# Kernel optimization log

Measured on AMD Instinct MI355X. Metric: run time of the kernel, lower is better.

Reference implementation:

```python
import jax, jax.numpy as jnp
import numpy as np

B, C, H, W = 8, 128, 64, 64
C8, C2 = C // 8, C // 2


def conv1x1(x, w, b):
    # x: [B,Cin,H,W], w: [Cout,Cin], b: [Cout]
    return jnp.einsum('bchw,oc->bohw', x, w) + b[None, :, None, None]


def maxpool2(x):
    # 2x2 stride-2 max pool on [B,C,H,W]
    b, c, h, w = x.shape
    return x.reshape(b, c, h // 2, 2, w // 2, 2).max(axis=(3, 5))


def setup_inputs() -> dict:
    key = jax.random.key(0)
    ks = jax.random.split(key, 10)
    s_in = 1.0 / np.sqrt(C)
    s_c2 = 1.0 / np.sqrt(C2)
    return {
        'x': jax.random.normal(ks[0], (B, C, H, W), dtype=jnp.float32),
        'w_theta': jax.random.uniform(ks[1], (C8, C), jnp.float32, -s_in, s_in),
        'b_theta': jax.random.uniform(ks[2], (C8,), jnp.float32, -s_in, s_in),
        'w_phi': jax.random.uniform(ks[3], (C8, C), jnp.float32, -s_in, s_in),
        'b_phi': jax.random.uniform(ks[4], (C8,), jnp.float32, -s_in, s_in),
        'w_g': jax.random.uniform(ks[5], (C2, C), jnp.float32, -s_in, s_in),
        'b_g': jax.random.uniform(ks[6], (C2,), jnp.float32, -s_in, s_in),
        'w_attn': jax.random.uniform(ks[7], (C, C2), jnp.float32, -s_c2, s_c2),
        'b_attn': jax.random.uniform(ks[8], (C,), jnp.float32, -s_c2, s_c2),
        'sigma': jnp.zeros((1,), dtype=jnp.float32),
    }


def reference(x, w_theta, b_theta, w_phi, b_phi, w_g, b_g, w_attn, b_attn, sigma):
    b, ch, h, w = x.shape
    n, m = h * w, (h * w) // 4
    theta = conv1x1(x, w_theta, b_theta).reshape(b, ch // 8, n)          # [B,C8,N]
    phi = maxpool2(conv1x1(x, w_phi, b_phi)).reshape(b, ch // 8, m)      # [B,C8,M]
    attn = jax.nn.softmax(jnp.einsum('bdn,bdm->bnm', theta, phi), axis=-1)  # [B,N,M]
    g = maxpool2(conv1x1(x, w_g, b_g)).reshape(b, ch // 2, m)            # [B,C2,M]
    attn_g = jnp.einsum('bcm,bnm->bcn', g, attn).reshape(b, ch // 2, h, w)
    attn_g = conv1x1(attn_g, w_attn, b_attn)
    return x + sigma[0] * attn_g
```

## Files before the change

### kernel.cpp

```cpp
#include <hip/hip_runtime.h>
#include <hip/hip_bf16.h>
#include <math.h>
#include <string.h>

#define Bn 8
#define Cn 128
#define Nn 4096
#define Mn 1024
#define C8n 16
#define C2n 64

typedef __attribute__((ext_vector_type(8))) short short8;
typedef __attribute__((ext_vector_type(4))) float floatx4;
typedef __attribute__((ext_vector_type(4))) unsigned short ushortx4;

__device__ __forceinline__ unsigned short f2bf(float f) {
    union { float f; unsigned u; } v; v.f = f;
    unsigned r = v.u + 0x7fff + ((v.u >> 16) & 1);
    return (unsigned short)(r >> 16);
}
__device__ __forceinline__ unsigned pk2(float a, float b) {
    __hip_bfloat162 h = __float22bfloat162_rn(make_float2(a, b));
    union { __hip_bfloat162 h2; unsigned u; } cv;
    cv.h2 = h;
    return cv.u;
}

__global__ __launch_bounds__(256) void k1_pre(
    const float* __restrict__ x,
    const float* __restrict__ w_theta, const float* __restrict__ b_theta,
    const float* __restrict__ w_phi,   const float* __restrict__ b_phi,
    const float* __restrict__ w_g,     const float* __restrict__ b_g,
    unsigned short* __restrict__ thA,
    unsigned short* __restrict__ phB,
    unsigned short* __restrict__ gB)
{
    __shared__ unsigned short wA[6 * 4 * 64 * 8];
    __shared__ unsigned short xB[8 * 4 * 64 * 8];
    __shared__ unsigned short pool[80][33];
    __shared__ float biases[96];

    const int t    = threadIdx.x;
    const int b    = blockIdx.x & 7;
    const int h2   = blockIdx.x >> 3;
    const int wv   = t >> 6;
    const int lane = t & 63;
    const int q    = lane >> 4;
    const int l15  = lane & 15;
    const float L2E = 1.4426950408889634f;

    if (t < 96)
        biases[t] = (t < 16) ? b_theta[t] * L2E
                  : (t < 32) ? b_phi[t - 16] : b_g[t - 32];

    #pragma unroll
    for (int k = 0; k < 12; ++k) {
        int u  = t + k * 256;
        int oc = u >> 5, c4 = u & 31;
        const float* src = (oc < 16) ? (w_theta + oc * Cn)
                         : (oc < 32) ? (w_phi + (oc - 16) * Cn)
                                     : (w_g + (oc - 32) * Cn);
        float4 wv4 = *(const float4*)(src + c4 * 4);
        float sc = (oc < 16) ? L2E : 1.f;
        int c = c4 * 4;
        int ot = oc >> 4, kc = c >> 5, qq = (c >> 3) & 3, jj = c & 7;
        uint2 pk = { pk2(wv4.x * sc, wv4.y * sc), pk2(wv4.z * sc, wv4.w * sc) };
        *(uint2*)(wA + (((ot * 4 + kc) * 64 + qq * 16 + (oc & 15)) * 8 + jj)) = pk;
    }

    const float* xb = x + (size_t)b * Cn * Nn + h2 * 128;
    #pragma unroll
    for (int k = 0; k < 16; ++k) {
        int u   = t + k * 256;
        int pos = u & 127, c4 = u >> 7;
        int c   = c4 * 4;
        float v0 = xb[(size_t)(c + 0) * Nn + pos];
        float v1 = xb[(size_t)(c + 1) * Nn + pos];
        float v2 = xb[(size_t)(c + 2) * Nn + pos];
        float v3 = xb[(size_t)(c + 3) * Nn + pos];
        int pt = pos >> 4, kc = c >> 5, qq = (c >> 3) & 3, jj = c & 7;
        uint2 pk = { pk2(v0, v1), pk2(v2, v3) };
        *(uint2*)(xB + (((pt * 4 + kc) * 64 + qq * 16 + (pos & 15)) * 8 + jj)) = pk;
    }
    __syncthreads();

    floatx4 acc[6][2];
    #pragma unroll
    for (int ot = 0; ot < 6; ++ot)
        #pragma unroll
        for (int p2 = 0; p2 < 2; ++p2) acc[ot][p2] = (floatx4){0.f, 0.f, 0.f, 0.f};

    #pragma unroll
    for (int kc = 0; kc < 4; ++kc) {
        short8 Bf0 = *(const short8*)(xB + ((wv * 4 + kc) * 64 + lane) * 8);
        short8 Bf1 = *(const short8*)(xB + (((wv + 4) * 4 + kc) * 64 + lane) * 8);
        #pragma unroll
        for (int ot = 0; ot < 6; ++ot) {
            short8 Af = *(const short8*)(wA + ((ot * 4 + kc) * 64 + lane) * 8);
            acc[ot][0] = __builtin_amdgcn_mfma_f32_16x16x32_bf16(Af, Bf0, acc[ot][0], 0, 0, 0);
            acc[ot][1] = __builtin_amdgcn_mfma_f32_16x16x32_bf16(Af, Bf1, acc[ot][1], 0, 0, 0);
        }
    }

    #pragma unroll
    for (int p2 = 0; p2 < 2; ++p2) {
        const int pt = wv + p2 * 4;
        float v0 = acc[0][p2][0] + biases[q * 4 + 0];
        float v1 = acc[0][p2][1] + biases[q * 4 + 1];
        float v2 = acc[0][p2][2] + biases[q * 4 + 2];
        float v3 = acc[0][p2][3] + biases[q * 4 + 3];
        uint2 pk = { pk2(v0, v1), pk2(v2, v3) };
        *(uint2*)(thA + ((((size_t)b * 256 + h2 * 8 + pt) * 2 + (q >> 1)) * 128
                         + l15 * 8 + (q & 1) * 4)) = pk;
    }

    #pragma unroll
    for (int ot = 1; ot < 6; ++ot) {
        #pragma unroll
        for (int r = 0; r < 4; ++r) {
            float vmax = fmaxf(acc[ot][0][r], acc[ot][1][r]);
            float pmax = fmaxf(vmax, __shfl_xor(vmax, 1, 64));
            if ((l15 & 1) == 0) {
                int oc = (ot - 1) * 16 + q * 4 + r;
                int w2 = wv * 8 + (l15 >> 1);
                pool[oc][w2] = f2bf(pmax + biases[16 + oc]);
            }
        }
    }
    __syncthreads();

    if (t < 64) {
        int w2h = t >> 5, ml = (t >> 1) & 15, dh = t & 1;
        int w2 = w2h * 16 + ml;
        ushortx4 lo, hi;
        #pragma unroll
        for (int j = 0; j < 4; ++j) { lo[j] = pool[dh * 8 + j][w2];
                                      hi[j] = pool[dh * 8 + 4 + j][w2]; }
        unsigned short* dst = phB + (((size_t)b * 64 + h2 * 2 + w2h) * 2 + dh) * 128 + ml * 8;
        *(ushortx4*)dst = lo;
        *(ushortx4*)(dst + 4) = hi;
    }
    {
        int c = t >> 2, sq = t & 3;
        ushortx4 lo, hi;
        #pragma unroll
        for (int j = 0; j < 8; ++j) {
            int w2 = (j & 1) * 16 + sq * 4 + (j >> 1);
            unsigned short v = pool[16 + c][w2];
            if (j < 4) lo[j] = v; else hi[j - 4] = v;
        }
        unsigned short* dst = gB + ((((size_t)b * 32 + h2) * 4 + (c >> 4)) * 4 + sq) * 128
                              + (c & 15) * 8;
        *(ushortx4*)dst = lo;
        *(ushortx4*)(dst + 4) = hi;
    }
}

__global__ __launch_bounds__(256, 2) void k2_attn(
    const float* __restrict__ x,
    const unsigned short* __restrict__ thA,
    const unsigned short* __restrict__ phB,
    const unsigned short* __restrict__ gB,
    const float* __restrict__ w_attn, const float* __restrict__ b_attn,
    const float* __restrict__ sigma_p,
    float* __restrict__ out)
{
    __shared__ float smem[18816];
    unsigned short* phis = (unsigned short*)smem;
    unsigned short* gs   = (unsigned short*)smem + 4096;
    char* Pall = (char*)smem + 40960;
    float* battn = (float*)((char*)smem + 74752);

    const int tid  = threadIdx.x;
    const int wave = tid >> 6;
    const int lane = tid & 63;
    const int q    = lane >> 4;
    const int l15  = lane & 15;
    const int b    = blockIdx.x & 7;
    const int n0   = (blockIdx.x >> 3) * 64;
    const int nw   = n0 + wave * 16;
    char* Pbase = Pall + wave * 8448;

    const float sg = sigma_p[0];

    short8 thf = {};
    if (q < 2)
        thf = *(const short8*)(thA + ((((size_t)b * 256 + (nw >> 4)) * 2 + q) * 16 + l15) * 8);

    floatx4 O[4];
    #pragma unroll
    for (int cs = 0; cs < 4; ++cs) O[cs] = (floatx4){0.f, 0.f, 0.f, 0.f};
    float L[4] = {0.f, 0.f, 0.f, 0.f};

    const float4* phib = (const float4*)(phB + (size_t)b * 64 * 256);
    const float4* gbb  = (const float4*)(gB + (size_t)b * 32 * 2048);

    float4 pre[10];
    #pragma unroll
    for (int k = 0; k < 10; ++k) {
        int i = tid + k * 256;
        pre[k] = (i < 512) ? phib[i] : gbb[i - 512];
    }

    for (int s = 0; s < 4; ++s) {
        __syncthreads();
        #pragma unroll
        for (int k = 0; k < 10; ++k) {
            int i = tid + k * 256;
            if (i < 512) ((float4*)smem)[i] = pre[k];
            else ((float4*)((char*)smem + 8192))[i - 512] = pre[k];
        }
        __syncthreads();
        if (s < 3) {
            #pragma unroll
            for (int k = 0; k < 10; ++k) {
                int i = tid + k * 256;
                pre[k] = (i < 512) ? phib[(s + 1) * 512 + i]
                                   : gbb[(s + 1) * 2048 + (i - 512)];
            }
        }

        #pragma unroll
        for (int g2 = 0; g2 < 8; ++g2) {
            short8 bf0 = {}, bf1 = {};
            if (q < 2) {
                bf0 = *(const short8*)(phis + (((2 * g2)     * 2 + q) * 16 + l15) * 8);
                bf1 = *(const short8*)(phis + (((2 * g2 + 1) * 2 + q) * 16 + l15) * 8);
            }
            floatx4 S0 = __builtin_amdgcn_mfma_f32_16x16x32_bf16(
                             thf, bf0, (floatx4){0.f, 0.f, 0.f, 0.f}, 0, 0, 0);
            floatx4 S1 = __builtin_amdgcn_mfma_f32_16x16x32_bf16(
                             thf, bf1, (floatx4){0.f, 0.f, 0.f, 0.f}, 0, 0, 0);
            #pragma unroll
            for (int r = 0; r < 4; ++r) {
                float pa = exp2f(S0[r]);
                float pb = exp2f(S1[r]);
                L[r] += pa + pb;
                *(unsigned*)(Pbase + (q * 4 + r) * 528 + g2 * 64 + l15 * 4) = pk2(pa, pb);
            }
        }

        #pragma unroll
        for (int ch = 0; ch < 8; ++ch) {
            short8 Af = *(const short8*)(Pbase + l15 * 528 + ch * 64 + q * 16);
            const unsigned short* gchunk = gs + ch * 2048;
            #pragma unroll
            for (int cs = 0; cs < 4; ++cs) {
                short8 Bf = *(const short8*)(gchunk + ((cs * 4 + q) * 16 + l15) * 8);
                O[cs] = __builtin_amdgcn_mfma_f32_16x16x32_bf16(Af, Bf, O[cs], 0, 0, 0);
            }
        }
    }

    #pragma unroll
    for (int d = 1; d <= 8; d <<= 1)
        #pragma unroll
        for (int r = 0; r < 4; ++r) L[r] += __shfl_xor(L[r], d, 64);

    __syncthreads();
    {
        unsigned short* wAe = (unsigned short*)smem;
        #pragma unroll
        for (int k = 0; k < 8; ++k) {
            int i = tid + k * 256;
            float4 wv = ((const float4*)w_attn)[i];
            int o = i >> 4, c = (i & 15) * 4;
            uint2 pk = { pk2(wv.x, wv.y), pk2(wv.z, wv.w) };
            *(uint2*)(wAe + ((o >> 4) * 2 + (c >> 5)) * 512 + (o & 15) * 32 + (c & 31)) = pk;
        }
        if (tid < 128) battn[tid] = b_attn[tid];
    }
    {
        float inv[4];
        #pragma unroll
        for (int r = 0; r < 4; ++r) inv[r] = 1.0f / L[r];
        unsigned short* Ob = (unsigned short*)Pbase;
        #pragma unroll
        for (int cs = 0; cs < 4; ++cs)
            #pragma unroll
            for (int r = 0; r < 4; ++r)
                Ob[(q * 4 + r) * 72 + cs * 16 + l15] = f2bf(O[cs][r] * inv[r]);
    }
    __syncthreads();

    {
        unsigned short* wAe = (unsigned short*)smem;
        unsigned short* Ob = (unsigned short*)Pbase;
        short8 B0 = *(const short8*)(Ob + l15 * 72 + q * 8);
        short8 B1 = *(const short8*)(Ob + l15 * 72 + 32 + q * 8);
        const float* xw = x   + (size_t)b * Cn * Nn + nw + l15;
        float*       ow = out + (size_t)b * Cn * Nn + nw + l15;
        #pragma unroll
        for (int ot = 0; ot < 8; ++ot) {
            short8 A0 = *(const short8*)(wAe + (ot * 2 + 0) * 512 + l15 * 32 + q * 8);
            short8 A1 = *(const short8*)(wAe + (ot * 2 + 1) * 512 + l15 * 32 + q * 8);
            floatx4 D = __builtin_amdgcn_mfma_f32_16x16x32_bf16(
                            A0, B0, (floatx4){0.f, 0.f, 0.f, 0.f}, 0, 0, 0);
            D = __builtin_amdgcn_mfma_f32_16x16x32_bf16(A1, B1, D, 0, 0, 0);
            #pragma unroll
            for (int r = 0; r < 4; ++r) {
                int o = ot * 16 + q * 4 + r;
                float v = D[r] + battn[o];
                ow[(size_t)o * Nn] = xw[(size_t)o * Nn] + sg * v;
            }
        }
    }
}

extern "C" void kernel_launch(void* const* d_in, const int* in_sizes, int n_in,
                              void* d_out, int out_size, void* d_ws, size_t ws_size,
                              hipStream_t stream) {
    const float* x       = (const float*)d_in[0];
    const float* w_theta = (const float*)d_in[1];
    const float* b_theta = (const float*)d_in[2];
    const float* w_phi   = (const float*)d_in[3];
    const float* b_phi   = (const float*)d_in[4];
    const float* w_g     = (const float*)d_in[5];
    const float* b_g     = (const float*)d_in[6];
    const float* w_attn  = (const float*)d_in[7];
    const float* b_attn  = (const float*)d_in[8];
    const float* sigma   = (const float*)d_in[9];
    float* out = (float*)d_out;

    unsigned short* thA = (unsigned short*)d_ws;
    unsigned short* phB = thA + 524288;
    unsigned short* gBp = phB + 131072;

    k1_pre<<<256, 256, 0, stream>>>(x, w_theta, b_theta, w_phi, b_phi,
                                    w_g, b_g, thA, phB, gBp);
    k2_attn<<<512, 256, 0, stream>>>(x, thA, phB, gBp, w_attn, b_attn, sigma, out);
}
```

Measured before the change: 129.9 us.

## Double-buffer phi/g tiles via direct global-to-LDS loads with smaller stages

Replaces the register-staged prefetch (global to registers, then a store to LDS) with __builtin_amdgcn_global_load_lds into two alternating LDS buffers. The M loop runs in 8 stages of 128 columns instead of 4 of 256, and the P scratch per wave shrinks to match. This removes the register pressure of the ten float4 prefetch registers and the second barrier per stage, and overlaps the next tile's load with compute. In exchange there are more loop iterations and barriers in total. There is no explicit vmcnt wait before reading the buffer, so correctness depends on how the compiler handles waits around __syncthreads.

```diff
diff --git a/kernel.cpp b/kernel.cpp
--- a/kernel.cpp
+++ b/kernel.cpp
@@ -13,6 +13,9 @@
 typedef __attribute__((ext_vector_type(8))) short short8;
 typedef __attribute__((ext_vector_type(4))) float floatx4;
 typedef __attribute__((ext_vector_type(4))) unsigned short ushortx4;
+
+typedef const __attribute__((address_space(1))) void gv_t;
+typedef __attribute__((address_space(3))) void lv_t;
 
 __device__ __forceinline__ unsigned short f2bf(float f) {
     union { float f; unsigned u; } v; v.f = f;
@@ -165,11 +168,11 @@
     const float* __restrict__ sigma_p,
     float* __restrict__ out)
 {
-    __shared__ float smem[18816];
-    unsigned short* phis = (unsigned short*)smem;
-    unsigned short* gs   = (unsigned short*)smem + 4096;
-    char* Pall = (char*)smem + 40960;
-    float* battn = (float*)((char*)smem + 74752);
+    __shared__ __attribute__((aligned(16))) char smem[58880];
+    char* buf0  = smem;
+    char* buf1  = smem + 20480;
+    char* Pall  = smem + 40960;
+    float* battn = (float*)(smem + 58368);
 
     const int tid  = threadIdx.x;
     const int wave = tid >> 6;
@@ -179,7 +182,7 @@
     const int b    = blockIdx.x & 7;
     const int n0   = (blockIdx.x >> 3) * 64;
     const int nw   = n0 + wave * 16;
-    char* Pbase = Pall + wave * 8448;
+    char* Pbase = Pall + wave * 4352;
 
     const float sg = sigma_p[0];
 
@@ -192,36 +195,33 @@
     for (int cs = 0; cs < 4; ++cs) O[cs] = (floatx4){0.f, 0.f, 0.f, 0.f};
     float L[4] = {0.f, 0.f, 0.f, 0.f};
 
-    const float4* phib = (const float4*)(phB + (size_t)b * 64 * 256);
-    const float4* gbb  = (const float4*)(gB + (size_t)b * 32 * 2048);
-
-    float4 pre[10];
-    #pragma unroll
-    for (int k = 0; k < 10; ++k) {
-        int i = tid + k * 256;
-        pre[k] = (i < 512) ? phib[i] : gbb[i - 512];
-    }
-
-    for (int s = 0; s < 4; ++s) {
+    const char* phb = (const char*)(phB + (size_t)b * 16384);
+    const char* gbb = (const char*)(gB  + (size_t)b * 65536);
+
+    for (int j = wave; j < 20; j += 4) {
+        const char* src = (j < 4) ? (phb + j * 1024) : (gbb + (j - 4) * 1024);
+        __builtin_amdgcn_global_load_lds((gv_t*)(src + lane * 16),
+                                         (lv_t*)(buf0 + j * 1024), 16, 0, 0);
+    }
+
+    for (int s = 0; s < 8; ++s) {
         __syncthreads();
-        #pragma unroll
-        for (int k = 0; k < 10; ++k) {
-            int i = tid + k * 256;
-            if (i < 512) ((float4*)smem)[i] = pre[k];
-            else ((float4*)((char*)smem + 8192))[i - 512] = pre[k];
-        }
-        __syncthreads();
-        if (s < 3) {
-            #pragma unroll
-            for (int k = 0; k < 10; ++k) {
-                int i = tid + k * 256;
-                pre[k] = (i < 512) ? phib[(s + 1) * 512 + i]
-                                   : gbb[(s + 1) * 2048 + (i - 512)];
-            }
-        }
-
-        #pragma unroll
-        for (int g2 = 0; g2 < 8; ++g2) {
+        if (s < 7) {
+            char* nbuf = (s & 1) ? buf0 : buf1;
+            const char* php = phb + (size_t)(s + 1) * 4096;
+            const char* gp  = gbb + (size_t)(s + 1) * 16384;
+            for (int j = wave; j < 20; j += 4) {
+                const char* src = (j < 4) ? (php + j * 1024) : (gp + (j - 4) * 1024);
+                __builtin_amdgcn_global_load_lds((gv_t*)(src + lane * 16),
+                                                 (lv_t*)(nbuf + j * 1024), 16, 0, 0);
+            }
+        }
+        const char* cbuf = (s & 1) ? buf1 : buf0;
+        const unsigned short* phis = (const unsigned short*)cbuf;
+        const unsigned short* gs   = (const unsigned short*)(cbuf + 4096);
+
+        #pragma unroll
+        for (int g2 = 0; g2 < 4; ++g2) {
             short8 bf0 = {}, bf1 = {};
             if (q < 2) {
                 bf0 = *(const short8*)(phis + (((2 * g2)     * 2 + q) * 16 + l15) * 8);
@@ -236,13 +236,13 @@
                 float pa = exp2f(S0[r]);
                 float pb = exp2f(S1[r]);
                 L[r] += pa + pb;
-                *(unsigned*)(Pbase + (q * 4 + r) * 528 + g2 * 64 + l15 * 4) = pk2(pa, pb);
-            }
-        }
-
-        #pragma unroll
-        for (int ch = 0; ch < 8; ++ch) {
-            short8 Af = *(const short8*)(Pbase + l15 * 528 + ch * 64 + q * 16);
+                *(unsigned*)(Pbase + (q * 4 + r) * 272 + g2 * 64 + l15 * 4) = pk2(pa, pb);
+            }
+        }
+
+        #pragma unroll
+        for (int ch = 0; ch < 4; ++ch) {
+            short8 Af = *(const short8*)(Pbase + l15 * 272 + ch * 64 + q * 16);
             const unsigned short* gchunk = gs + ch * 2048;
             #pragma unroll
             for (int cs = 0; cs < 4; ++cs) {
```

Result: faster. 115.2 us (-11.3%).
